# Optimization experiments

Measured on AMD Instinct MI355X. Metric: run time of the kernel, lower is better.

## Reference

```python
import jax, jax.numpy as jnp
import numpy as np

N_NODES = 100000
N_EDGES = 1600000
IN, HID, OUT = 128, 128, 64


def setup_inputs() -> dict:
    key = jax.random.key(0)
    ks = jax.random.split(key, 12)
    x = jax.random.normal(ks[0], (N_NODES, IN), dtype=jnp.float32)
    src = jax.random.randint(ks[1], (N_EDGES,), 0, N_NODES, dtype=jnp.int32)
    dst = jax.random.randint(ks[2], (N_EDGES,), 0, N_NODES, dtype=jnp.int32)

    def lin(k, fan_in, fan_out):
        return jax.random.normal(k, (fan_in, fan_out), dtype=jnp.float32) / jnp.sqrt(jnp.float32(fan_in))

    return {
        "x": x, "src": src, "dst": dst,
        "w_self_0": lin(ks[3], IN, HID), "w_neigh_0": lin(ks[4], IN, HID), "b_0": jnp.zeros((HID,), jnp.float32),
        "w_self_1": lin(ks[5], HID, HID), "w_neigh_1": lin(ks[6], HID, HID), "b_1": jnp.zeros((HID,), jnp.float32),
        "w_self_2": lin(ks[7], HID, OUT), "w_neigh_2": lin(ks[8], HID, OUT), "b_2": jnp.zeros((OUT,), jnp.float32),
    }


def reference(x, src, dst, w_self_0, w_neigh_0, b_0, w_self_1, w_neigh_1, b_1, w_self_2, w_neigh_2, b_2):
    n = x.shape[0]
    # in-degree per dst node; zero-degree nodes keep aggregated 0 (clamp avoids div-by-0)
    deg = jax.ops.segment_sum(jnp.ones_like(dst, dtype=x.dtype), dst, num_segments=n)
    inv_deg = (1.0 / jnp.maximum(deg, 1.0))[:, None]

    def sage_layer(h, w_s, w_n, b):
        # irregular gather of src features, segment-mean over dst
        agg = jax.ops.segment_sum(h[src], dst, num_segments=n) * inv_deg
        return h @ w_s + agg @ w_n + b

    h = jax.nn.relu(sage_layer(x, w_self_0, w_neigh_0, b_0))   # dropout = identity (eval)
    h = jax.nn.relu(sage_layer(h, w_self_1, w_neigh_1, b_1))
    return sage_layer(h, w_self_2, w_neigh_2, b_2)
```

## Files before the change

### kernel.cpp

```cpp
#include <hip/hip_runtime.h>


#define NN 100000
#define NE 1600000
#define BSH 7
#define BND 128
#define NB  782
#define NBLKS 256
#define EPB ((NE + NBLKS - 1) / NBLKS)
#define STOT (NB * NBLKS)
#define NSB ((STOT + 1023) / 1024)
#define GEMM_BLOCKS 1563

typedef __attribute__((ext_vector_type(8))) short short8;
typedef __attribute__((ext_vector_type(4))) float f32x4;
typedef unsigned int uint;
typedef unsigned short ushort;

__device__ inline ushort f2bf(float f) {
    uint u = __float_as_uint(f);
    u += 0x7FFFu + ((u >> 16) & 1u);
    return (ushort)(u >> 16);
}
__device__ inline float bf_lo(uint w) { return __uint_as_float(w << 16); }
__device__ inline float bf_hi(uint w) { return __uint_as_float(w & 0xFFFF0000u); }

template<int NCS, int NCN, bool XF32, bool ABF>
__device__ void gemm_body(int bid, int tid,
    const void* __restrict__ Hv, const ushort* __restrict__ Wf,
    const float* __restrict__ bias, void* __restrict__ Av, ushort* __restrict__ Bt)
{
    constexpr int NCT = (NCS + NCN) / 16;
    const int g = (bid * 256 + tid) >> 6;
    if (g >= NN / 16) return;
    const int lane = tid & 63;
    const int m = lane & 15;
    const int q = lane >> 4;

    short8 af[4];
    if (XF32) {
        const float* hp = (const float*)Hv + (size_t)(g * 16 + m) * 128;
        #pragma unroll
        for (int kt = 0; kt < 4; ++kt) {
            const float4 f0 = *(const float4*)(hp + kt * 32 + q * 8);
            const float4 f1 = *(const float4*)(hp + kt * 32 + q * 8 + 4);
            short8 v;
            v[0] = (short)f2bf(f0.x); v[1] = (short)f2bf(f0.y);
            v[2] = (short)f2bf(f0.z); v[3] = (short)f2bf(f0.w);
            v[4] = (short)f2bf(f1.x); v[5] = (short)f2bf(f1.y);
            v[6] = (short)f2bf(f1.z); v[7] = (short)f2bf(f1.w);
            af[kt] = v;
        }
    } else {
        const short8* hp = (const short8*)((const ushort*)Hv + (size_t)(g * 16 + m) * 128);
        #pragma unroll
        for (int kt = 0; kt < 4; ++kt) af[kt] = hp[kt * 4 + q];
    }

    f32x4 acc[NCT];
    #pragma unroll
    for (int i = 0; i < NCT; ++i) acc[i] = (f32x4){0.f, 0.f, 0.f, 0.f};

    const short8* wp = (const short8*)Wf;
    #pragma unroll
    for (int ct = 0; ct < NCT; ++ct) {
        #pragma unroll
        for (int kt = 0; kt < 4; ++kt) {
            const short8 bf = wp[(ct * 4 + kt) * 64 + lane];
            acc[ct] = __builtin_amdgcn_mfma_f32_16x16x32_bf16(af[kt], bf, acc[ct], 0, 0, 0);
        }
    }

    const int r0 = g * 16 + q * 4;
    #pragma unroll
    for (int ct = 0; ct < NCS / 16; ++ct) {
        const int c = ct * 16 + m;
        const float bv = bias[c];
        #pragma unroll
        for (int r = 0; r < 4; ++r) {
            const float v = acc[ct][r] + bv;
            if (ABF) ((ushort*)Av)[(size_t)(r0 + r) * NCS + c] = f2bf(v);
            else     ((float*) Av)[(size_t)(r0 + r) * NCS + c] = v;
        }
    }
    #pragma unroll
    for (int ct = NCS / 16; ct < NCT; ++ct) {
        const int c = ct * 16 + m - NCS;
        #pragma unroll
        for (int r = 0; r < 4; ++r)
            Bt[(size_t)(r0 + r) * NCN + c] = f2bf(acc[ct][r]);
    }
}

template<int NCS, int NCN, bool XF32, bool ABF>
__global__ __launch_bounds__(256) void gemm_mfma_k(
    const void* __restrict__ Hv, const ushort* __restrict__ Wf,
    const float* __restrict__ bias, void* __restrict__ Av, ushort* __restrict__ Bt)
{
    gemm_body<NCS, NCN, XF32, ABF>(blockIdx.x, threadIdx.x, Hv, Wf, bias, Av, Bt);
}

__global__ __launch_bounds__(256) void phist_pack_k(
    const int* __restrict__ dst, int* __restrict__ histG,
    const float* __restrict__ ws0, const float* __restrict__ wn0, ushort* __restrict__ wf0,
    const float* __restrict__ ws1, const float* __restrict__ wn1, ushort* __restrict__ wf1,
    const float* __restrict__ ws2, const float* __restrict__ wn2, ushort* __restrict__ wf2)
{
    __shared__ int h[NB];
    const int t = threadIdx.x;
    if (blockIdx.x < NBLKS) {
        for (int i = t; i < NB; i += 256) h[i] = 0;
        __syncthreads();
        const int blk = blockIdx.x;
        const int e0 = blk * EPB;
        const int e1 = min(e0 + EPB, NE);
        for (int e = e0 + t; e < e1; e += 256)
            atomicAdd(&h[dst[e] >> BSH], 1);
        __syncthreads();
        for (int i = t; i < NB; i += 256)
            histG[i * NBLKS + blk] = h[i];
        return;
    }
    const int b = blockIdx.x - NBLKS;
    const float *ws, *wn; ushort* wf; int ncs, idx;
    if (b < 16)      { ws = ws0; wn = wn0; wf = wf0; ncs = 128; idx = b * 256 + t; }
    else if (b < 32) { ws = ws1; wn = wn1; wf = wf1; ncs = 128; idx = (b - 16) * 256 + t; }
    else             { ws = ws2; wn = wn2; wf = wf2; ncs = 64;  idx = (b - 32) * 256 + t; }
    const int total = (2 * ncs / 16) * 4 * 64;
    if (idx >= total) return;
    const int l = idx & 63;
    const int f = idx >> 6;
    const int kt = f & 3;
    const int ct = f >> 2;
    const int n = ct * 16 + (l & 15);
    const int k0 = kt * 32 + (l >> 4) * 8;
    uint w[4];
    #pragma unroll
    for (int p = 0; p < 4; ++p) {
        const int k = k0 + p * 2;
        float v0, v1;
        if (n < ncs) { v0 = ws[k * ncs + n];         v1 = ws[(k + 1) * ncs + n]; }
        else         { v0 = wn[k * ncs + (n - ncs)]; v1 = wn[(k + 1) * ncs + (n - ncs)]; }
        w[p] = (uint)f2bf(v0) | ((uint)f2bf(v1) << 16);
    }
    uint4 o; o.x = w[0]; o.y = w[1]; o.z = w[2]; o.w = w[3];
    ((uint4*)wf)[idx] = o;
}

__global__ __launch_bounds__(256) void scan1_k(int* __restrict__ data, int* __restrict__ blksum) {
    __shared__ int lds[256];
    const int t = threadIdx.x;
    const int base = blockIdx.x * 1024 + t * 4;
    int v[4];
    #pragma unroll
    for (int i = 0; i < 4; ++i) {
        const int idx = base + i;
        v[i] = (idx < STOT) ? data[idx] : 0;
    }
    const int s = v[0] + v[1] + v[2] + v[3];
    lds[t] = s;
    __syncthreads();
    #pragma unroll
    for (int off = 1; off < 256; off <<= 1) {
        const int cur = lds[t];
        const int y = (t >= off) ? lds[t - off] : 0;
        __syncthreads();
        lds[t] = cur + y;
        __syncthreads();
    }
    const int incl = lds[t];
    if (t == 255) blksum[blockIdx.x] = incl;
    int run = incl - s;
    #pragma unroll
    for (int i = 0; i < 4; ++i) {
        const int idx = base + i;
        if (idx < STOT) data[idx] = run;
        run += v[i];
    }
}

__global__ __launch_bounds__(256) void scan3_k(int* __restrict__ data, const int* __restrict__ blksum) {
    __shared__ int lds[256];
    const int t = threadIdx.x;
    lds[t] = (t < NSB) ? blksum[t] : 0;
    __syncthreads();
    #pragma unroll
    for (int off = 1; off < 256; off <<= 1) {
        const int cur = lds[t];
        const int y = (t >= off) ? lds[t - off] : 0;
        __syncthreads();
        lds[t] = cur + y;
        __syncthreads();
    }
    const int add = (blockIdx.x == 0) ? 0 : lds[blockIdx.x - 1];
    const int base = blockIdx.x * 1024 + t * 4;
    #pragma unroll
    for (int i = 0; i < 4; ++i) {
        const int idx = base + i;
        if (idx < STOT) data[idx] += add;
    }
}

__global__ __launch_bounds__(256) void pscatter_gemm0_k(
    const int* __restrict__ src, const int* __restrict__ dst,
    const int* __restrict__ histG, int* __restrict__ pb,
    const float* __restrict__ x, const ushort* __restrict__ wf0,
    const float* __restrict__ b0, ushort* __restrict__ Abf, ushort* __restrict__ Bt)
{
    __shared__ int wc[NB];
    const int t = threadIdx.x;
    if (blockIdx.x < NBLKS) {
        const int blk = blockIdx.x;
        for (int i = t; i < NB; i += 256) wc[i] = histG[i * NBLKS + blk];
        __syncthreads();
        const int e0 = blk * EPB;
        const int e1 = min(e0 + EPB, NE);
        for (int e = e0 + t; e < e1; e += 256) {
            const int d = dst[e];
            const int pos = atomicAdd(&wc[d >> BSH], 1);
            pb[pos] = (src[e] << BSH) | (d & (BND - 1));
        }
        return;
    }
    gemm_body<128, 128, true, true>(blockIdx.x - NBLKS, t, x, wf0, b0, Abf, Bt);
}

__global__ __launch_bounds__(256) void bucket_place_k(const int* __restrict__ histG,
                                                      const int* __restrict__ pb,
                                                      int* __restrict__ row,
                                                      int* __restrict__ esrc) {
    __shared__ int cnt[BND], wc[BND], excl[BND], scan[BND];
    const int b = blockIdx.x;
    const int t = threadIdx.x;
    if (t < BND) { cnt[t] = 0; wc[t] = 0; }
    __syncthreads();
    const int s0 = histG[b * NBLKS];
    const int s1 = (b + 1 < NB) ? histG[(b + 1) * NBLKS] : NE;
    for (int e = s0 + t; e < s1; e += 256)
        atomicAdd(&cnt[pb[e] & (BND - 1)], 1);
    __syncthreads();
    if (t < BND) scan[t] = cnt[t];
    __syncthreads();
    for (int off = 1; off < BND; off <<= 1) {
        int nv = 0;
        if (t < BND) {
            nv = scan[t];
            if (t >= off) nv += scan[t - off];
        }
        __syncthreads();
        if (t < BND) scan[t] = nv;
        __syncthreads();
    }
    if (t < BND) {
        const int ex = scan[t] - cnt[t];
        excl[t] = ex;
        const int node = b * BND + t;
        if (node <= NN) row[node] = s0 + ex;
    }
    __syncthreads();
    for (int e = s0 + t; e < s1; e += 256) {
        const int p = pb[e];
        const int dl = p & (BND - 1);
        const int pos = s0 + excl[dl] + atomicAdd(&wc[dl], 1);
        esrc[pos] = p >> BSH;
    }
}

__global__ __launch_bounds__(256) void agg128_k(
    const int* __restrict__ row, const int* __restrict__ esrc,
    const ushort* __restrict__ Bt, const ushort* __restrict__ Abf, ushort* __restrict__ Hb)
{
    const int w = (blockIdx.x * 256 + threadIdx.x) >> 6;
    const int half = (threadIdx.x >> 5) & 1;
    const int ln = threadIdx.x & 31;
    const int node = w * 2 + half;
    if (node >= NN) return;
    const int e0 = row[node];
    const int e1 = row[node + 1];
    const uint2* B = (const uint2*)Bt;
    float a0 = 0.f, a1 = 0.f, a2 = 0.f, a3 = 0.f;
    int e = e0;
    for (; e + 8 <= e1; e += 8) {
        int s[8];
        #pragma unroll
        for (int j = 0; j < 8; ++j) s[j] = esrc[e + j];
        uint2 v[8];
        #pragma unroll
        for (int j = 0; j < 8; ++j) v[j] = B[(size_t)s[j] * 32 + ln];
        #pragma unroll
        for (int j = 0; j < 8; ++j) {
            a0 += bf_lo(v[j].x); a1 += bf_hi(v[j].x);
            a2 += bf_lo(v[j].y); a3 += bf_hi(v[j].y);
        }
    }
    for (; e + 2 <= e1; e += 2) {
        const int s0 = esrc[e], s1 = esrc[e + 1];
        const uint2 v0 = B[(size_t)s0 * 32 + ln];
        const uint2 v1 = B[(size_t)s1 * 32 + ln];
        a0 += bf_lo(v0.x) + bf_lo(v1.x); a1 += bf_hi(v0.x) + bf_hi(v1.x);
        a2 += bf_lo(v0.y) + bf_lo(v1.y); a3 += bf_hi(v0.y) + bf_hi(v1.y);
    }
    if (e < e1) {
        const uint2 v = B[(size_t)esrc[e] * 32 + ln];
        a0 += bf_lo(v.x); a1 += bf_hi(v.x);
        a2 += bf_lo(v.y); a3 += bf_hi(v.y);
    }
    const int deg = e1 - e0;
    const float invd = (deg > 0) ? 1.0f / (float)deg : 0.0f;
    const uint2 aw = ((const uint2*)Abf)[(size_t)node * 32 + ln];
    const float v0 = fmaxf(bf_lo(aw.x) + a0 * invd, 0.f);
    const float v1 = fmaxf(bf_hi(aw.x) + a1 * invd, 0.f);
    const float v2 = fmaxf(bf_lo(aw.y) + a2 * invd, 0.f);
    const float v3 = fmaxf(bf_hi(aw.y) + a3 * invd, 0.f);
    uint2 o;
    o.x = (uint)f2bf(v0) | ((uint)f2bf(v1) << 16);
    o.y = (uint)f2bf(v2) | ((uint)f2bf(v3) << 16);
    ((uint2*)Hb)[(size_t)node * 32 + ln] = o;
}

__global__ __launch_bounds__(256) void agg64_k(
    const int* __restrict__ row, const int* __restrict__ esrc,
    const ushort* __restrict__ Bt, float* __restrict__ out)
{
    const int node = (blockIdx.x * 256 + threadIdx.x) >> 4;
    const int ln = threadIdx.x & 15;
    if (node >= NN) return;
    const int e0 = row[node];
    const int e1 = row[node + 1];
    const uint2* B = (const uint2*)Bt;
    float a0 = 0.f, a1 = 0.f, a2 = 0.f, a3 = 0.f;
    int e = e0;
    for (; e + 8 <= e1; e += 8) {
        int s[8];
        #pragma unroll
        for (int j = 0; j < 8; ++j) s[j] = esrc[e + j];
        uint2 v[8];
        #pragma unroll
        for (int j = 0; j < 8; ++j) v[j] = B[(size_t)s[j] * 16 + ln];
        #pragma unroll
        for (int j = 0; j < 8; ++j) {
            a0 += bf_lo(v[j].x); a1 += bf_hi(v[j].x);
            a2 += bf_lo(v[j].y); a3 += bf_hi(v[j].y);
        }
    }
    for (; e + 2 <= e1; e += 2) {
        const int s0 = esrc[e], s1 = esrc[e + 1];
        const uint2 v0 = B[(size_t)s0 * 16 + ln];
        const uint2 v1 = B[(size_t)s1 * 16 + ln];
        a0 += bf_lo(v0.x) + bf_lo(v1.x); a1 += bf_hi(v0.x) + bf_hi(v1.x);
        a2 += bf_lo(v0.y) + bf_lo(v1.y); a3 += bf_hi(v0.y) + bf_hi(v1.y);
    }
    if (e < e1) {
        const uint2 v = B[(size_t)esrc[e] * 16 + ln];
        a0 += bf_lo(v.x); a1 += bf_hi(v.x);
        a2 += bf_lo(v.y); a3 += bf_hi(v.y);
    }
    const int deg = e1 - e0;
    const float invd = (deg > 0) ? 1.0f / (float)deg : 0.0f;
    float4* op = (float4*)(out + (size_t)node * 64 + ln * 4);
    float4 o = *op;
    o.x += a0 * invd; o.y += a1 * invd;
    o.z += a2 * invd; o.w += a3 * invd;
    *op = o;
}

__device__ inline float4 relu4f(float4 v) {
    v.x = fmaxf(v.x, 0.f); v.y = fmaxf(v.y, 0.f);
    v.z = fmaxf(v.z, 0.f); v.w = fmaxf(v.w, 0.f);
    return v;
}
template<int NCOL, bool RELU_IN, bool BIAS>
__global__ __launch_bounds__(256) void gemm_k(
    const float* in, const float* __restrict__ W,
    const float* __restrict__ bias, float* out)
{
    constexpr int K = 128;
    constexpr int QUADS = NCOL / 4;
    constexpr int G = 256 / QUADS;
    constexpr int RPT = 32 / G;
    __shared__ float Wlds[K * NCOL];
    {
        const float4* Wg = reinterpret_cast<const float4*>(W);
        float4* Wl = reinterpret_cast<float4*>(Wlds);
        #pragma unroll
        for (int i = 0; i < K * NCOL / 4 / 256; ++i)
            Wl[threadIdx.x + i * 256] = Wg[threadIdx.x + i * 256];
    }
    __syncthreads();
    const int tx = threadIdx.x % QUADS;
    const int ty = threadIdx.x / QUADS;
    const int row0 = blockIdx.x * 32;
    const float* rp[RPT];
    #pragma unroll
    for (int i = 0; i < RPT; ++i) rp[i] = in + (size_t)(row0 + ty + i * G) * K;
    float acc[RPT][4];
    #pragma unroll
    for (int i = 0; i < RPT; ++i) acc[i][0] = acc[i][1] = acc[i][2] = acc[i][3] = 0.f;
    #pragma unroll 2
    for (int kc = 0; kc < K; kc += 4) {
        float4 h4[RPT];
        #pragma unroll
        for (int i = 0; i < RPT; ++i) {
            h4[i] = *reinterpret_cast<const float4*>(rp[i] + kc);
            if (RELU_IN) h4[i] = relu4f(h4[i]);
        }
        #pragma unroll
        for (int kk = 0; kk < 4; ++kk) {
            const float4 w4 = *reinterpret_cast<const float4*>(&Wlds[(kc + kk) * NCOL + tx * 4]);
            #pragma unroll
            for (int i = 0; i < RPT; ++i) {
                const float hv = (&h4[i].x)[kk];
                acc[i][0] = fmaf(hv, w4.x, acc[i][0]);
                acc[i][1] = fmaf(hv, w4.y, acc[i][1]);
                acc[i][2] = fmaf(hv, w4.z, acc[i][2]);
                acc[i][3] = fmaf(hv, w4.w, acc[i][3]);
            }
        }
    }
    float4 b4 = make_float4(0.f, 0.f, 0.f, 0.f);
    if (BIAS) b4 = *reinterpret_cast<const float4*>(&bias[tx * 4]);
    #pragma unroll
    for (int i = 0; i < RPT; ++i) {
        const int r = row0 + ty + i * G;
        float4 o;
        o.x = acc[i][0] + b4.x; o.y = acc[i][1] + b4.y;
        o.z = acc[i][2] + b4.z; o.w = acc[i][3] + b4.w;
        *reinterpret_cast<float4*>(&out[(size_t)r * NCOL + tx * 4]) = o;
    }
}
__global__ void deg_k(const int* __restrict__ dst, float* __restrict__ deg, int E) {
    const int i = blockIdx.x * blockDim.x + threadIdx.x;
    if (i < E) atomicAdd(&deg[dst[i]], 1.0f);
}
__global__ void inv_k(float* deg, int n) {
    const int i = blockIdx.x * blockDim.x + threadIdx.x;
    if (i < n) deg[i] = 1.0f / fmaxf(deg[i], 1.0f);
}
__global__ __launch_bounds__(256) void scatter128_k(
    const int* __restrict__ src, const int* __restrict__ dst,
    const float* __restrict__ inv, const float* __restrict__ B, float* A, int E) {
    const int lane = threadIdx.x & 63;
    int w = (blockIdx.x * 256 + threadIdx.x) >> 6;
    const int nw = (gridDim.x * 256) >> 6;
    for (int e = w; e < E; e += nw) {
        const int s = src[e], d = dst[e];
        const float sc = inv[d];
        const float2 v = *reinterpret_cast<const float2*>(&B[(size_t)s * 128 + lane * 2]);
        atomicAdd(&A[(size_t)d * 128 + lane * 2    ], v.x * sc);
        atomicAdd(&A[(size_t)d * 128 + lane * 2 + 1], v.y * sc);
    }
}
__global__ __launch_bounds__(256) void scatter64_k(
    const int* __restrict__ src, const int* __restrict__ dst,
    const float* __restrict__ inv, const float* __restrict__ B, float* A, int E) {
    const int lane = threadIdx.x & 63;
    int w = (blockIdx.x * 256 + threadIdx.x) >> 6;
    const int nw = (gridDim.x * 256) >> 6;
    for (int e = w; e < E; e += nw) {
        const int s = src[e], d = dst[e];
        atomicAdd(&A[(size_t)d * 64 + lane], B[(size_t)s * 64 + lane] * inv[d]);
    }
}

extern "C" void kernel_launch(void* const* d_in, const int* in_sizes, int n_in,
                              void* d_out, int out_size, void* d_ws, size_t ws_size,
                              hipStream_t stream) {
    const float* x   = (const float*)d_in[0];
    const int*   src = (const int*)  d_in[1];
    const int*   dst = (const int*)  d_in[2];
    const float* ws0 = (const float*)d_in[3];
    const float* wn0 = (const float*)d_in[4];
    const float* b0  = (const float*)d_in[5];
    const float* ws1 = (const float*)d_in[6];
    const float* wn1 = (const float*)d_in[7];
    const float* b1  = (const float*)d_in[8];
    const float* ws2 = (const float*)d_in[9];
    const float* wn2 = (const float*)d_in[10];
    const float* b2  = (const float*)d_in[11];
    float* out = (float*)d_out;

    const size_t O_BLK  = 4096;
    const size_t O_ROW  = 16384;
    const size_t O_WF0  = 417792;
    const size_t O_WF1  = 483328;
    const size_t O_WF2  = 548864;
    const size_t O_ESRC = 581632;
    const size_t O_PB   = 6983680;
    const size_t O_HIST = 13385728;
    const size_t O_A    = 14286848;
    const size_t O_BT   = 39890944;
    const size_t O_HB   = 65495040;
    const size_t NEED   = 91095040;

    if (ws_size >= NEED) {
        int*    blks  = (int*)   ((char*)d_ws + O_BLK);
        int*    row   = (int*)   ((char*)d_ws + O_ROW);
        ushort* wf0   = (ushort*)((char*)d_ws + O_WF0);
        ushort* wf1   = (ushort*)((char*)d_ws + O_WF1);
        ushort* wf2   = (ushort*)((char*)d_ws + O_WF2);
        int*    esrc  = (int*)   ((char*)d_ws + O_ESRC);
        int*    pb    = (int*)   ((char*)d_ws + O_PB);
        int*    histG = (int*)   ((char*)d_ws + O_HIST);
        ushort* Abf   = (ushort*)((char*)d_ws + O_A);
        ushort* Bt    = (ushort*)((char*)d_ws + O_BT);
        ushort* Hb    = (ushort*)((char*)d_ws + O_HB);

        phist_pack_k<<<NBLKS + 40, 256, 0, stream>>>(dst, histG,
            ws0, wn0, wf0, ws1, wn1, wf1, ws2, wn2, wf2);
        scan1_k<<<NSB, 256, 0, stream>>>(histG, blks);
        scan3_k<<<NSB, 256, 0, stream>>>(histG, blks);
        pscatter_gemm0_k<<<NBLKS + GEMM_BLOCKS, 256, 0, stream>>>(
            src, dst, histG, pb, x, wf0, b0, Abf, Bt);
        bucket_place_k<<<NB, 256, 0, stream>>>(histG, pb, row, esrc);

        const int AGG128_BLOCKS = (NN / 2 + 3) / 4;
        const int AGG64_BLOCKS  = (NN + 63) / 64;
        const int A64B = (NN + 15) / 16;

        agg128_k<<<AGG128_BLOCKS, 256, 0, stream>>>(row, esrc, Bt, Abf, Hb);
        gemm_mfma_k<128, 128, false, true ><<<GEMM_BLOCKS, 256, 0, stream>>>(Hb, wf1, b1, Abf, Bt);
        agg128_k<<<AGG128_BLOCKS, 256, 0, stream>>>(row, esrc, Bt, Abf, Hb);
        gemm_mfma_k<64, 64, false, false><<<GEMM_BLOCKS, 256, 0, stream>>>(Hb, wf2, b2, out, Bt);
        agg64_k<<<A64B, 256, 0, stream>>>(row, esrc, Bt, out);
        (void)AGG64_BLOCKS;
    } else {
        float* inv = (float*)d_ws;
        float* H0  = (float*)((char*)d_ws + (1u << 20));
        float* Bf  = H0 + (size_t)NN * 128;
        const int GB = NN / 32;
        const int SC_BLOCKS = 4096;
        hipMemsetAsync(inv, 0, NN * sizeof(float), stream);
        deg_k<<<(NE + 255) / 256, 256, 0, stream>>>(dst, inv, NE);
        inv_k<<<(NN + 255) / 256, 256, 0, stream>>>(inv, NN);
        gemm_k<128, false, false><<<GB, 256, 0, stream>>>(x, wn0, nullptr, Bf);
        gemm_k<128, false, true ><<<GB, 256, 0, stream>>>(x, ws0, b0, H0);
        scatter128_k<<<SC_BLOCKS, 256, 0, stream>>>(src, dst, inv, Bf, H0, NE);
        gemm_k<128, true, false><<<GB, 256, 0, stream>>>(H0, wn1, nullptr, Bf);
        gemm_k<128, true, true ><<<GB, 256, 0, stream>>>(H0, ws1, b1, H0);
        scatter128_k<<<SC_BLOCKS, 256, 0, stream>>>(src, dst, inv, Bf, H0, NE);
        gemm_k<64, true, false><<<GB, 256, 0, stream>>>(H0, wn2, nullptr, Bf);
        gemm_k<64, true, true ><<<GB, 256, 0, stream>>>(H0, ws2, b2, out);
        scatter64_k<<<SC_BLOCKS, 256, 0, stream>>>(src, dst, inv, Bf, out, NE);
    }
}
```

Baseline: 394.5 us.

## Widen gather loads, stage GEMM weights in LDS, double histogram blocks

```diff
diff --git a/kernel.cpp b/kernel.cpp
--- a/kernel.cpp
+++ b/kernel.cpp
@@ -6,10 +6,11 @@
 #define BSH 7
 #define BND 128
 #define NB  782
-#define NBLKS 256
+#define NBLKS 512
 #define EPB ((NE + NBLKS - 1) / NBLKS)
 #define STOT (NB * NBLKS)
-#define NSB ((STOT + 1023) / 1024)
+#define SCAN_E 2048
+#define NSB ((STOT + SCAN_E - 1) / SCAN_E)
 #define GEMM_BLOCKS 1563
 
 typedef __attribute__((ext_vector_type(8))) short short8;
@@ -25,21 +26,31 @@
 __device__ inline float bf_lo(uint w) { return __uint_as_float(w << 16); }
 __device__ inline float bf_hi(uint w) { return __uint_as_float(w & 0xFFFF0000u); }
 
-template<int NCS, int NCN, bool XF32, bool ABF>
-__device__ void gemm_body(int bid, int tid,
+template<int NCS, int NCN, bool XF32, bool ABF, bool WLDS>
+__device__ void gemm_body(int wid, int tid, int nthr,
     const void* __restrict__ Hv, const ushort* __restrict__ Wf,
     const float* __restrict__ bias, void* __restrict__ Av, ushort* __restrict__ Bt)
 {
     constexpr int NCT = (NCS + NCN) / 16;
-    const int g = (bid * 256 + tid) >> 6;
-    if (g >= NN / 16) return;
+    const short8* wp;
+    if constexpr (WLDS) {
+        __shared__ short8 wl[NCT * 4 * 64];
+        uint4* dl = (uint4*)wl;
+        const uint4* sg = (const uint4*)Wf;
+        for (int i = tid; i < NCT * 4 * 64; i += nthr) dl[i] = sg[i];
+        __syncthreads();
+        wp = wl;
+    } else {
+        wp = (const short8*)Wf;
+    }
+    if (wid >= NN / 16) return;
     const int lane = tid & 63;
     const int m = lane & 15;
     const int q = lane >> 4;
 
     short8 af[4];
     if (XF32) {
-        const float* hp = (const float*)Hv + (size_t)(g * 16 + m) * 128;
+        const float* hp = (const float*)Hv + (size_t)(wid * 16 + m) * 128;
         #pragma unroll
         for (int kt = 0; kt < 4; ++kt) {
             const float4 f0 = *(const float4*)(hp + kt * 32 + q * 8);
@@ -52,7 +63,7 @@
             af[kt] = v;
         }
     } else {
-        const short8* hp = (const short8*)((const ushort*)Hv + (size_t)(g * 16 + m) * 128);
+        const short8* hp = (const short8*)((const ushort*)Hv + (size_t)(wid * 16 + m) * 128);
         #pragma unroll
         for (int kt = 0; kt < 4; ++kt) af[kt] = hp[kt * 4 + q];
     }
@@ -61,7 +72,6 @@
     #pragma unroll
     for (int i = 0; i < NCT; ++i) acc[i] = (f32x4){0.f, 0.f, 0.f, 0.f};
 
-    const short8* wp = (const short8*)Wf;
     #pragma unroll
     for (int ct = 0; ct < NCT; ++ct) {
         #pragma unroll
@@ -71,7 +81,7 @@
         }
     }
 
-    const int r0 = g * 16 + q * 4;
+    const int r0 = wid * 16 + q * 4;
     #pragma unroll
     for (int ct = 0; ct < NCS / 16; ++ct) {
         const int c = ct * 16 + m;
@@ -93,11 +103,12 @@
 }
 
 template<int NCS, int NCN, bool XF32, bool ABF>
-__global__ __launch_bounds__(256) void gemm_mfma_k(
+__global__ __launch_bounds__(512) void gemm_mfma_k(
     const void* __restrict__ Hv, const ushort* __restrict__ Wf,
     const float* __restrict__ bias, void* __restrict__ Av, ushort* __restrict__ Bt)
 {
-    gemm_body<NCS, NCN, XF32, ABF>(blockIdx.x, threadIdx.x, Hv, Wf, bias, Av, Bt);
+    gemm_body<NCS, NCN, XF32, ABF, true>(
+        (blockIdx.x * 512 + threadIdx.x) >> 6, threadIdx.x, 512, Hv, Wf, bias, Av, Bt);
 }
 
 __global__ __launch_bounds__(256) void phist_pack_k(
@@ -150,14 +161,15 @@
 __global__ __launch_bounds__(256) void scan1_k(int* __restrict__ data, int* __restrict__ blksum) {
     __shared__ int lds[256];
     const int t = threadIdx.x;
-    const int base = blockIdx.x * 1024 + t * 4;
-    int v[4];
-    #pragma unroll
-    for (int i = 0; i < 4; ++i) {
+    const int base = blockIdx.x * SCAN_E + t * 8;
+    int v[8];
+    int s = 0;
+    #pragma unroll
+    for (int i = 0; i < 8; ++i) {
         const int idx = base + i;
         v[i] = (idx < STOT) ? data[idx] : 0;
-    }
-    const int s = v[0] + v[1] + v[2] + v[3];
+        s += v[i];
+    }
     lds[t] = s;
     __syncthreads();
     #pragma unroll
@@ -172,7 +184,7 @@
     if (t == 255) blksum[blockIdx.x] = incl;
     int run = incl - s;
     #pragma unroll
-    for (int i = 0; i < 4; ++i) {
+    for (int i = 0; i < 8; ++i) {
         const int idx = base + i;
         if (idx < STOT) data[idx] = run;
         run += v[i];
@@ -193,9 +205,9 @@
         __syncthreads();
     }
     const int add = (blockIdx.x == 0) ? 0 : lds[blockIdx.x - 1];
-    const int base = blockIdx.x * 1024 + t * 4;
-    #pragma unroll
-    for (int i = 0; i < 4; ++i) {
+    const int base = blockIdx.x * SCAN_E + t * 8;
+    #pragma unroll
+    for (int i = 0; i < 8; ++i) {
         const int idx = base + i;
         if (idx < STOT) data[idx] += add;
     }
@@ -222,7 +234,8 @@
         }
         return;
     }
-    gemm_body<128, 128, true, true>(blockIdx.x - NBLKS, t, x, wf0, b0, Abf, Bt);
+    gemm_body<128, 128, true, true, false>(
+        ((blockIdx.x - NBLKS) * 256 + t) >> 6, t, 256, x, wf0, b0, Abf, Bt);
 }
 
 __global__ __launch_bounds__(256) void bucket_place_k(const int* __restrict__ histG,
@@ -270,98 +283,132 @@
     const int* __restrict__ row, const int* __restrict__ esrc,
     const ushort* __restrict__ Bt, const ushort* __restrict__ Abf, ushort* __restrict__ Hb)
 {
-    const int w = (blockIdx.x * 256 + threadIdx.x) >> 6;
-    const int half = (threadIdx.x >> 5) & 1;
-    const int ln = threadIdx.x & 31;
-    const int node = w * 2 + half;
-    if (node >= NN) return;
-    const int e0 = row[node];
-    const int e1 = row[node + 1];
-    const uint2* B = (const uint2*)Bt;
-    float a0 = 0.f, a1 = 0.f, a2 = 0.f, a3 = 0.f;
-    int e = e0;
-    for (; e + 8 <= e1; e += 8) {
-        int s[8];
-        #pragma unroll
-        for (int j = 0; j < 8; ++j) s[j] = esrc[e + j];
-        uint2 v[8];
-        #pragma unroll
-        for (int j = 0; j < 8; ++j) v[j] = B[(size_t)s[j] * 32 + ln];
-        #pragma unroll
-        for (int j = 0; j < 8; ++j) {
-            a0 += bf_lo(v[j].x); a1 += bf_hi(v[j].x);
-            a2 += bf_lo(v[j].y); a3 += bf_hi(v[j].y);
-        }
-    }
-    for (; e + 2 <= e1; e += 2) {
-        const int s0 = esrc[e], s1 = esrc[e + 1];
-        const uint2 v0 = B[(size_t)s0 * 32 + ln];
-        const uint2 v1 = B[(size_t)s1 * 32 + ln];
-        a0 += bf_lo(v0.x) + bf_lo(v1.x); a1 += bf_hi(v0.x) + bf_hi(v1.x);
-        a2 += bf_lo(v0.y) + bf_lo(v1.y); a3 += bf_hi(v0.y) + bf_hi(v1.y);
-    }
-    if (e < e1) {
-        const uint2 v = B[(size_t)esrc[e] * 32 + ln];
-        a0 += bf_lo(v.x); a1 += bf_hi(v.x);
-        a2 += bf_lo(v.y); a3 += bf_hi(v.y);
-    }
-    const int deg = e1 - e0;
-    const float invd = (deg > 0) ? 1.0f / (float)deg : 0.0f;
-    const uint2 aw = ((const uint2*)Abf)[(size_t)node * 32 + ln];
-    const float v0 = fmaxf(bf_lo(aw.x) + a0 * invd, 0.f);
-    const float v1 = fmaxf(bf_hi(aw.x) + a1 * invd, 0.f);
-    const float v2 = fmaxf(bf_lo(aw.y) + a2 * invd, 0.f);
-    const float v3 = fmaxf(bf_hi(aw.y) + a3 * invd, 0.f);
-    uint2 o;
-    o.x = (uint)f2bf(v0) | ((uint)f2bf(v1) << 16);
-    o.y = (uint)f2bf(v2) | ((uint)f2bf(v3) << 16);
-    ((uint2*)Hb)[(size_t)node * 32 + ln] = o;
-}
-
-__global__ __launch_bounds__(256) void agg64_k(
-    const int* __restrict__ row, const int* __restrict__ esrc,
-    const ushort* __restrict__ Bt, float* __restrict__ out)
-{
     const int node = (blockIdx.x * 256 + threadIdx.x) >> 4;
     const int ln = threadIdx.x & 15;
     if (node >= NN) return;
     const int e0 = row[node];
     const int e1 = row[node + 1];
-    const uint2* B = (const uint2*)Bt;
+    const uint4* B = (const uint4*)Bt;
     float a0 = 0.f, a1 = 0.f, a2 = 0.f, a3 = 0.f;
+    float a4 = 0.f, a5 = 0.f, a6 = 0.f, a7 = 0.f;
     int e = e0;
     for (; e + 8 <= e1; e += 8) {
         int s[8];
         #pragma unroll
         for (int j = 0; j < 8; ++j) s[j] = esrc[e + j];
-        uint2 v[8];
+        uint4 v[8];
         #pragma unroll
         for (int j = 0; j < 8; ++j) v[j] = B[(size_t)s[j] * 16 + ln];
         #pragma unroll
         for (int j = 0; j < 8; ++j) {
             a0 += bf_lo(v[j].x); a1 += bf_hi(v[j].x);
             a2 += bf_lo(v[j].y); a3 += bf_hi(v[j].y);
-        }
-    }
-    for (; e + 2 <= e1; e += 2) {
-        const int s0 = esrc[e], s1 = esrc[e + 1];
-        const uint2 v0 = B[(size_t)s0 * 16 + ln];
-        const uint2 v1 = B[(size_t)s1 * 16 + ln];
-        a0 += bf_lo(v0.x) + bf_lo(v1.x); a1 += bf_hi(v0.x) + bf_hi(v1.x);
-        a2 += bf_lo(v0.y) + bf_lo(v1.y); a3 += bf_hi(v0.y) + bf_hi(v1.y);
-    }
-    if (e < e1) {
-        const uint2 v = B[(size_t)esrc[e] * 16 + ln];
+            a4 += bf_lo(v[j].z); a5 += bf_hi(v[j].z);
+            a6 += bf_lo(v[j].w); a7 += bf_hi(v[j].w);
+        }
+    }
+    if (e + 4 <= e1) {
+        int s[4];
+        #pragma unroll
+        for (int j = 0; j < 4; ++j) s[j] = esrc[e + j];
+        uint4 v[4];
+        #pragma unroll
+        for (int j = 0; j < 4; ++j) v[j] = B[(size_t)s[j] * 16 + ln];
+        #pragma unroll
+        for (int j = 0; j < 4; ++j) {
+            a0 += bf_lo(v[j].x); a1 += bf_hi(v[j].x);
+            a2 += bf_lo(v[j].y); a3 += bf_hi(v[j].y);
+            a4 += bf_lo(v[j].z); a5 += bf_hi(v[j].z);
+            a6 += bf_lo(v[j].w); a7 += bf_hi(v[j].w);
+        }
+        e += 4;
+    }
+    for (; e < e1; ++e) {
+        const uint4 v = B[(size_t)esrc[e] * 16 + ln];
         a0 += bf_lo(v.x); a1 += bf_hi(v.x);
         a2 += bf_lo(v.y); a3 += bf_hi(v.y);
+        a4 += bf_lo(v.z); a5 += bf_hi(v.z);
+        a6 += bf_lo(v.w); a7 += bf_hi(v.w);
     }
     const int deg = e1 - e0;
     const float invd = (deg > 0) ? 1.0f / (float)deg : 0.0f;
-    float4* op = (float4*)(out + (size_t)node * 64 + ln * 4);
-    float4 o = *op;
-    o.x += a0 * invd; o.y += a1 * invd;
-    o.z += a2 * invd; o.w += a3 * invd;
-    *op = o;
+    const uint4 aw = ((const uint4*)Abf)[(size_t)node * 16 + ln];
+    const float v0 = fmaxf(bf_lo(aw.x) + a0 * invd, 0.f);
+    const float v1 = fmaxf(bf_hi(aw.x) + a1 * invd, 0.f);
+    const float v2 = fmaxf(bf_lo(aw.y) + a2 * invd, 0.f);
+    const float v3 = fmaxf(bf_hi(aw.y) + a3 * invd, 0.f);
+    const float v4 = fmaxf(bf_lo(aw.z) + a4 * invd, 0.f);
+    const float v5 = fmaxf(bf_hi(aw.z) + a5 * invd, 0.f);
+    const float v6 = fmaxf(bf_lo(aw.w) + a6 * invd, 0.f);
+    const float v7 = fmaxf(bf_hi(aw.w) + a7 * invd, 0.f);
+    uint4 o;
+    o.x = (uint)f2bf(v0) | ((uint)f2bf(v1) << 16);
+    o.y = (uint)f2bf(v2) | ((uint)f2bf(v3) << 16);
+    o.z = (uint)f2bf(v4) | ((uint)f2bf(v5) << 16);
+    o.w = (uint)f2bf(v6) | ((uint)f2bf(v7) << 16);
+    ((uint4*)Hb)[(size_t)node * 16 + ln] = o;
+}
+
+__global__ __launch_bounds__(256) void agg64_k(
+    const int* __restrict__ row, const int* __restrict__ esrc,
+    const ushort* __restrict__ Bt, float* __restrict__ out)
+{
+    const int node = (blockIdx.x * 256 + threadIdx.x) >> 3;
+    const int ln = threadIdx.x & 7;
+    if (node >= NN) return;
+    const int e0 = row[node];
+    const int e1 = row[node + 1];
+    const uint4* B = (const uint4*)Bt;
+    float a0 = 0.f, a1 = 0.f, a2 = 0.f, a3 = 0.f;
+    float a4 = 0.f, a5 = 0.f, a6 = 0.f, a7 = 0.f;
+    int e = e0;
+    for (; e + 8 <= e1; e += 8) {
+        int s[8];
+        #pragma unroll
+        for (int j = 0; j < 8; ++j) s[j] = esrc[e + j];
+        uint4 v[8];
+        #pragma unroll
+        for (int j = 0; j < 8; ++j) v[j] = B[(size_t)s[j] * 8 + ln];
+        #pragma unroll
+        for (int j = 0; j < 8; ++j) {
+            a0 += bf_lo(v[j].x); a1 += bf_hi(v[j].x);
+            a2 += bf_lo(v[j].y); a3 += bf_hi(v[j].y);
+            a4 += bf_lo(v[j].z); a5 += bf_hi(v[j].z);
+            a6 += bf_lo(v[j].w); a7 += bf_hi(v[j].w);
+        }
+    }
+    if (e + 4 <= e1) {
+        int s[4];
+        #pragma unroll
+        for (int j = 0; j < 4; ++j) s[j] = esrc[e + j];
+        uint4 v[4];
+        #pragma unroll
+        for (int j = 0; j < 4; ++j) v[j] = B[(size_t)s[j] * 8 + ln];
+        #pragma unroll
+        for (int j = 0; j < 4; ++j) {
+            a0 += bf_lo(v[j].x); a1 += bf_hi(v[j].x);
+            a2 += bf_lo(v[j].y); a3 += bf_hi(v[j].y);
+            a4 += bf_lo(v[j].z); a5 += bf_hi(v[j].z);
+            a6 += bf_lo(v[j].w); a7 += bf_hi(v[j].w);
+        }
+        e += 4;
+    }
+    for (; e < e1; ++e) {
+        const uint4 v = B[(size_t)esrc[e] * 8 + ln];
+        a0 += bf_lo(v.x); a1 += bf_hi(v.x);
+        a2 += bf_lo(v.y); a3 += bf_hi(v.y);
+        a4 += bf_lo(v.z); a5 += bf_hi(v.z);
+        a6 += bf_lo(v.w); a7 += bf_hi(v.w);
+    }
+    const int deg = e1 - e0;
+    const float invd = (deg > 0) ? 1.0f / (float)deg : 0.0f;
+    float4* op = (float4*)(out + (size_t)node * 64 + ln * 8);
+    float4 o0 = op[0], o1 = op[1];
+    o0.x += a0 * invd; o0.y += a1 * invd;
+    o0.z += a2 * invd; o0.w += a3 * invd;
+    o1.x += a4 * invd; o1.y += a5 * invd;
+    o1.z += a6 * invd; o1.w += a7 * invd;
+    op[0] = o0; op[1] = o1;
 }
 
 __device__ inline float4 relu4f(float4 v) {
@@ -486,7 +533,6 @@
     const size_t O_WF2  = 548864;
     const size_t O_ESRC = 581632;
     const size_t O_PB   = 6983680;
-    const size_t O_HIST = 13385728;
     const size_t O_A    = 14286848;
     const size_t O_BT   = 39890944;
     const size_t O_HB   = 65495040;
@@ -500,10 +546,10 @@
         ushort* wf2   = (ushort*)((char*)d_ws + O_WF2);
         int*    esrc  = (int*)   ((char*)d_ws + O_ESRC);
         int*    pb    = (int*)   ((char*)d_ws + O_PB);
-        int*    histG = (int*)   ((char*)d_ws + O_HIST);
         ushort* Abf   = (ushort*)((char*)d_ws + O_A);
         ushort* Bt    = (ushort*)((char*)d_ws + O_BT);
         ushort* Hb    = (ushort*)((char*)d_ws + O_HB);
+        int*    histG = (int*)   ((char*)d_ws + O_HB);
 
         phist_pack_k<<<NBLKS + 40, 256, 0, stream>>>(dst, histG,
             ws0, wn0, wf0, ws1, wn1, wf1, ws2, wn2, wf2);
@@ -513,16 +559,15 @@
             src, dst, histG, pb, x, wf0, b0, Abf, Bt);
         bucket_place_k<<<NB, 256, 0, stream>>>(histG, pb, row, esrc);
 
-        const int AGG128_BLOCKS = (NN / 2 + 3) / 4;
-        const int AGG64_BLOCKS  = (NN + 63) / 64;
-        const int A64B = (NN + 15) / 16;
+        const int AGG128_BLOCKS = (NN + 15) / 16;
+        const int AGG64_BLOCKS  = (NN + 31) / 32;
+        const int GEMM512_BLOCKS = (NN / 16 + 7) / 8;
 
         agg128_k<<<AGG128_BLOCKS, 256, 0, stream>>>(row, esrc, Bt, Abf, Hb);
-        gemm_mfma_k<128, 128, false, true ><<<GEMM_BLOCKS, 256, 0, stream>>>(Hb, wf1, b1, Abf, Bt);
+        gemm_mfma_k<128, 128, false, true ><<<GEMM512_BLOCKS, 512, 0, stream>>>(Hb, wf1, b1, Abf, Bt);
         agg128_k<<<AGG128_BLOCKS, 256, 0, stream>>>(row, esrc, Bt, Abf, Hb);
-        gemm_mfma_k<64, 64, false, false><<<GEMM_BLOCKS, 256, 0, stream>>>(Hb, wf2, b2, out, Bt);
-        agg64_k<<<A64B, 256, 0, stream>>>(row, esrc, Bt, out);
-        (void)AGG64_BLOCKS;
+        gemm_mfma_k<64, 64, false, false><<<GEMM512_BLOCKS, 512, 0, stream>>>(Hb, wf2, b2, out, Bt);
+        agg64_k<<<AGG64_BLOCKS, 256, 0, stream>>>(row, esrc, Bt, out);
     } else {
         float* inv = (float*)d_ws;
         float* H0  = (float*)((char*)d_ws + (1u << 20));
```

New measurement: 376.5 us. -4.6%, faster.
